# Performance work log

Hardware: AMD Instinct MI355X
Metric: run time of the kernel (lower is better)

Reference implementation:

```python
import jax, jax.numpy as jnp
import numpy as np

VOCAB_SIZES = [100003, 100019, 100043, 100049, 100057, 100069, 100103, 100109,
               100129, 100151, 100153, 100169, 100183, 100189, 100193, 100207]
OFFSETS = np.cumsum([0] + VOCAB_SIZES[:-1]).astype(np.int32)  # per-head offsets into shared table
B, S, G, C = 2, 2048, 4, 2048        # batch, seq, hc_mult branches, base_emb_dim
H, DH = 16, 64                        # total hash heads, dim_per_head
ENGRAM_DIM = H * DH                   # 1024 = num_orders * dim_per_ngram
K, DIL = 4, 3                         # conv kernel_size, dilation = max_ngram_size


def setup_inputs() -> dict:
  key = jax.random.key(0)
  ks = jax.random.split(key, 8)
  total_vocab = sum(VOCAB_SIZES)
  return {
      "hidden_states": jax.random.normal(ks[0], (B, S, G, C), jnp.float32),
      "hash_input_ids": jax.random.randint(ks[1], (B, S, H), 0, min(VOCAB_SIZES), jnp.int32),
      "emb_table": jax.random.normal(ks[2], (total_vocab, DH), jnp.float32) * 0.02,
      "key_w": jax.random.normal(ks[3], (G, ENGRAM_DIM, C), jnp.float32) / np.sqrt(ENGRAM_DIM),
      "key_b": jnp.zeros((G, C), jnp.float32),
      "k_scale": jnp.ones((G, C), jnp.float32) + 0.02 * jax.random.normal(ks[4], (G, C), jnp.float32),
      "q_scale": jnp.ones((G, C), jnp.float32) + 0.02 * jax.random.normal(ks[5], (G, C), jnp.float32),
      "value_w": jax.random.normal(ks[6], (ENGRAM_DIM, C), jnp.float32) / np.sqrt(ENGRAM_DIM),
      "value_b": jnp.zeros((C,), jnp.float32),
      "conv_scale": jnp.ones((G, C), jnp.float32),
      "conv_w": jax.random.normal(ks[7], (K, G * C), jnp.float32) * 0.25,  # depthwise taps
  }


def _rmsnorm(x, scale, eps):
  var = jnp.mean(jnp.square(x), axis=-1, keepdims=True)
  return x * jax.lax.rsqrt(var + eps) * scale


def reference(hidden_states, hash_input_ids, emb_table, key_w, key_b,
              k_scale, q_scale, value_w, value_b, conv_scale, conv_w):
  # 1. Retrieve: offset-shifted multi-head embedding gather
  ids = hash_input_ids + jnp.asarray(OFFSETS)            # (B,S,H)
  emb = emb_table[ids].reshape(B, S, ENGRAM_DIM)         # (B,S,H*DH)
  # 2. Gate: per-branch key projections + RMSNorms, signed-sqrt sigmoid gate
  keys = jnp.einsum('bse,geo->bsgo', emb, key_w) + key_b  # (B,S,G,C)
  k = _rmsnorm(keys, k_scale, 1e-6)
  q = _rmsnorm(hidden_states, q_scale, 1e-6)
  qk = jnp.einsum('bsgc,bsgc->bsg', q, k) / jnp.sqrt(jnp.float32(C))
  gate_logits = jnp.sqrt(jnp.maximum(jnp.abs(qk), 1e-6)) * jnp.sign(qk)
  gates = jax.nn.sigmoid(gate_logits)                    # (B,S,G)
  value = emb @ value_w + value_b                        # (B,S,C)
  v = gates[..., None] * value[:, :, None, :]            # (B,S,G,C)
  # 3. Mix: ShortConv = SiLU(depthwise causal dilated Conv1D(RMSNorm(v)))
  xn = _rmsnorm(v, conv_scale, 1e-5).reshape(B, S, G * C)
  pad = (K - 1) * DIL                                    # causal left pad = 9
  xp = jnp.pad(xn, ((0, 0), (pad, 0), (0, 0)))
  y = sum(xp[:, j * DIL:j * DIL + S, :] * conv_w[j] for j in range(K))
  y = jax.nn.silu(y).reshape(B, S, G, C)
  return v + y
```

## Files before the change

kernel.cpp:

```cpp
#include <hip/hip_runtime.h>
#include <cstdint>
#include <cstddef>

typedef __attribute__((ext_vector_type(8))) __bf16 bf16x8;
typedef __attribute__((ext_vector_type(4))) float f32x4;
typedef __attribute__((ext_vector_type(4))) unsigned short u16x4;
typedef __attribute__((ext_vector_type(8))) unsigned short u16x8;

static constexpr int Bz = 2, Sz = 2048, Gz = 4, Cz = 2048;
static constexpr int Hh = 16, EDz = 1024;
static constexpr int Tz = Bz * Sz;
static constexpr int NALL = Gz * Cz + Cz;

__constant__ int OFF16[16] = {0, 100003, 200022, 300065, 400114, 500171, 600240,
                              700343, 800452, 900581, 1000732, 1100885, 1201054,
                              1301237, 1401426, 1501619};

__device__ __forceinline__ float bf2f(unsigned short s) {
  union { unsigned u; float f; } x; x.u = ((unsigned)s) << 16; return x.f;
}
__device__ __forceinline__ unsigned short f2bf(float f) {
  union { float f; unsigned u; } x; x.f = f;
  unsigned r = x.u + 0x7fff + ((x.u >> 16) & 1);
  return (unsigned short)(r >> 16);
}

__global__ __launch_bounds__(256) void k_bias(const float* __restrict__ key_b,
                                              const float* __restrict__ value_b,
                                              float* __restrict__ bias) {
  int n = blockIdx.x * 256 + threadIdx.x;
  bias[n] = (n < Gz * Cz) ? key_b[n] : value_b[n - Gz * Cz];
}

__global__ __launch_bounds__(256) void k_prepw(const float* __restrict__ key_w,
                                               const float* __restrict__ value_w,
                                               unsigned short* __restrict__ Wt) {
  __shared__ float tile[32][33];
  const int mat = blockIdx.y;
  const int ot = blockIdx.x & 63, kt = blockIdx.x >> 6;
  const float* src = (mat < 4) ? (key_w + (size_t)mat * EDz * Cz) : value_w;
  const int tx = threadIdx.x & 31, ty = threadIdx.x >> 5;
#pragma unroll
  for (int i = 0; i < 4; i++)
    tile[ty + i * 8][tx] = src[(size_t)(kt * 32 + ty + i * 8) * Cz + ot * 32 + tx];
  __syncthreads();
#pragma unroll
  for (int i = 0; i < 4; i++)
    Wt[(size_t)(mat * Cz + ot * 32 + ty + i * 8) * EDz + kt * 32 + tx] =
        f2bf(tile[tx][ty + i * 8]);
}

__global__ __launch_bounds__(256) void k_gather(const int* __restrict__ ids,
                                                const float* __restrict__ table,
                                                unsigned short* __restrict__ emb) {
  const int t = blockIdx.x;
  const int tid = threadIdx.x;
  const int h = tid >> 4;
  const int d = (tid & 15) * 4;
  const long row = (long)(ids[t * Hh + h] + OFF16[h]);
  f32x4 v = *reinterpret_cast<const f32x4*>(table + row * 64 + d);
  u16x4 o;
#pragma unroll
  for (int i = 0; i < 4; i++) o[i] = f2bf(v[i]);
  *reinterpret_cast<u16x4*>(emb + (size_t)t * EDz + tid * 4) = o;
}

#define GEMM_BAR  asm volatile("s_barrier" ::: "memory")
#define GEMM_V4   asm volatile("s_waitcnt vmcnt(4)" ::: "memory")

__global__ __launch_bounds__(512, 2) void k_gemm8(const unsigned short* __restrict__ A,
                                                  const unsigned short* __restrict__ Bw,
                                                  const float* __restrict__ bias,
                                                  unsigned short* __restrict__ Cm) {
  __shared__ unsigned short s_lds[65536];
  char* lds_c = (char*)s_lds;

  const int tid = threadIdx.x;
  const int wid = tid >> 6, lane = tid & 63;
  const int wr = wid >> 2, wc = wid & 3;

  const int bid = blockIdx.x;
  const int swz = (bid & 7) * 80 + (bid >> 3);
  const int bm = swz / 40, bn = swz % 40;
  const int m0 = bm * 256, n0 = bn * 256;

  int rq[2], kq[2];
#pragma unroll
  for (int q = 0; q < 2; q++) {
    int x = q * 8192 + wid * 1024 + lane * 16;
    int y = x ^ (((x >> 9) & 1) << 5);
    rq[q] = ((y >> 11) & 7) * 16 + ((y >> 6) & 15);
    kq[q] = ((y >> 10) & 1) * 32 + ((y >> 1) & 31);
  }
  const int rdb = (((lane & 15) << 6) + ((lane >> 4) << 4)) ^ (((lane >> 3) & 1) << 5);

  const unsigned short* Arow0 = A + (size_t)m0 * EDz;
  const unsigned short* Arow1 = A + (size_t)(m0 + 128) * EDz;
  const unsigned short* Brow0 = Bw + (size_t)n0 * EDz;
  const unsigned short* Brow1 = Bw + (size_t)(n0 + 128) * EDz;

  auto STAGE = [&](const unsigned short* grow, int ldsOff, int kt) {
#pragma unroll
    for (int q = 0; q < 2; q++) {
      const unsigned short* src = grow + (size_t)rq[q] * EDz + kt * 64 + kq[q];
      __builtin_amdgcn_global_load_lds(
          (const __attribute__((address_space(1))) void*)src,
          (__attribute__((address_space(3))) void*)(lds_c + ldsOff + q * 8192 + wid * 1024),
          16, 0, 0);
    }
  };

  f32x4 acc[8][4] = {};
  bf16x8 Af[4][2], Bl[2][2], Bh[2][2];

  auto RD_A = [&](int buf, int msel) {
    const char* p = lds_c + buf * 32768 + wr * 16384 + rdb;
#pragma unroll
    for (int m = 0; m < 4; m++)
#pragma unroll
      for (int ks = 0; ks < 2; ks++)
        Af[m][ks] = *reinterpret_cast<const bf16x8*>(p + (msel * 4 + m) * 2048 + ks * 1024);
  };
  auto RD_B = [&](int buf, int nsel, bf16x8 (&Bf)[2][2]) {
    const char* p = lds_c + 65536 + buf * 32768 + (wc >> 1) * 16384 + (wc & 1) * 8192 + rdb;
#pragma unroll
    for (int n = 0; n < 2; n++)
#pragma unroll
      for (int ks = 0; ks < 2; ks++)
        Bf[n][ks] = *reinterpret_cast<const bf16x8*>(p + (nsel * 2 + n) * 2048 + ks * 1024);
  };
  auto MM = [&](int msel, int nsel, bf16x8 (&Bf)[2][2]) {
    __builtin_amdgcn_s_setprio(1);
#pragma unroll
    for (int m = 0; m < 4; m++)
#pragma unroll
      for (int n = 0; n < 2; n++)
#pragma unroll
        for (int ks = 0; ks < 2; ks++)
          acc[msel * 4 + m][nsel * 2 + n] = __builtin_amdgcn_mfma_f32_16x16x32_bf16(
              Af[m][ks], Bf[n][ks], acc[msel * 4 + m][nsel * 2 + n], 0, 0, 0);
    __builtin_amdgcn_s_setprio(0);
  };

  STAGE(Arow0, 0,             0);
  STAGE(Arow1, 16384,         0);
  STAGE(Brow0, 65536,         0);
  STAGE(Brow1, 65536 + 16384, 0);
  STAGE(Brow0, 65536 + 32768,         1);
  STAGE(Brow1, 65536 + 32768 + 16384, 1);
  GEMM_V4;
  GEMM_BAR;

  for (int i = 0; i < 8; ++i) {
    const int o  = 2 * i + 1;
    const int t2 = (2 * i + 2 > 15) ? 15 : 2 * i + 2;
    const int t3 = (2 * i + 3 > 15) ? 15 : 2 * i + 3;
    RD_A(0, 0); RD_B(0, 0, Bl);
    STAGE(Arow0, 32768, o);
    GEMM_BAR; MM(0, 0, Bl); GEMM_BAR;
    RD_B(0, 1, Bh);
    STAGE(Arow1, 32768 + 16384, o);
    GEMM_BAR; MM(0, 1, Bh); GEMM_BAR;
    RD_A(0, 1);
    STAGE(Brow0, 65536, t2);
    GEMM_BAR; MM(1, 0, Bl); GEMM_BAR;
    STAGE(Brow1, 65536 + 16384, t2);
    GEMM_V4;
    GEMM_BAR; MM(1, 1, Bh); GEMM_BAR;
    RD_A(1, 0); RD_B(1, 0, Bl);
    STAGE(Arow0, 0, t2);
    GEMM_BAR; MM(0, 0, Bl); GEMM_BAR;
    RD_B(1, 1, Bh);
    STAGE(Arow1, 16384, t2);
    GEMM_BAR; MM(0, 1, Bh); GEMM_BAR;
    RD_A(1, 1);
    STAGE(Brow0, 65536 + 32768, t3);
    GEMM_BAR; MM(1, 0, Bl); GEMM_BAR;
    STAGE(Brow1, 65536 + 32768 + 16384, t3);
    GEMM_V4;
    GEMM_BAR; MM(1, 1, Bh); GEMM_BAR;
  }

#pragma unroll
  for (int mrep = 0; mrep < 8; mrep++) {
    const int row = m0 + wr * 128 + mrep * 16 + (lane >> 4) * 4;
#pragma unroll
    for (int nrep = 0; nrep < 4; nrep++) {
      const int col = n0 + wc * 64 + nrep * 16 + (lane & 15);
      const float bb = bias[col];
#pragma unroll
      for (int t = 0; t < 4; t++)
        Cm[(size_t)(row + t) * NALL + col] = f2bf(acc[mrep][nrep][t] + bb);
    }
  }
}

__global__ __launch_bounds__(256) void k_gate(const float* __restrict__ hidden,
                                              const unsigned short* __restrict__ kv,
                                              const float* __restrict__ k_scale,
                                              const float* __restrict__ q_scale,
                                              float* __restrict__ gates,
                                              float* __restrict__ rstd) {
  const int t = blockIdx.x;
  const int tid = threadIdx.x;
  const int lane = tid & 63, w = tid >> 6;
  const int c0 = tid * 8;
  __shared__ float sred[4][13];
  float val[8];
  {
    bf16x8 raw = *reinterpret_cast<const bf16x8*>(kv + (size_t)t * NALL + Gz * Cz + c0);
#pragma unroll
    for (int i = 0; i < 8; i++) val[i] = (float)raw[i];
  }
  float p[13];
#pragma unroll
  for (int j = 0; j < 13; j++) p[j] = 0.f;
#pragma unroll
  for (int i = 0; i < 8; i++) p[12] += val[i] * val[i];
#pragma unroll
  for (int g = 0; g < 4; g++) {
    const float* qp = hidden + (size_t)t * (Gz * Cz) + g * Cz + c0;
    f32x4 q0 = *reinterpret_cast<const f32x4*>(qp);
    f32x4 q1 = *reinterpret_cast<const f32x4*>(qp + 4);
    bf16x8 kr = *reinterpret_cast<const bf16x8*>(kv + (size_t)t * NALL + g * Cz + c0);
    f32x4 qs0 = *reinterpret_cast<const f32x4*>(q_scale + g * Cz + c0);
    f32x4 qs1 = *reinterpret_cast<const f32x4*>(q_scale + g * Cz + c0 + 4);
    f32x4 ks0 = *reinterpret_cast<const f32x4*>(k_scale + g * Cz + c0);
    f32x4 ks1 = *reinterpret_cast<const f32x4*>(k_scale + g * Cz + c0 + 4);
#pragma unroll
    for (int i = 0; i < 8; i++) {
      float qi = (i < 4) ? q0[i] : q1[i - 4];
      float ki = (float)kr[i];
      float qsi = (i < 4) ? qs0[i] : qs1[i - 4];
      float ksi = (i < 4) ? ks0[i] : ks1[i - 4];
      p[3 * g + 0] += qi * qi;
      p[3 * g + 1] += ki * ki;
      p[3 * g + 2] += qi * qsi * ki * ksi;
    }
  }
#pragma unroll
  for (int j = 0; j < 13; j++) {
    float x = p[j];
    for (int off = 32; off; off >>= 1) x += __shfl_down(x, off);
    if (lane == 0) sred[w][j] = x;
  }
  __syncthreads();
  if (tid != 0) return;
  float f[13];
#pragma unroll
  for (int j = 0; j < 13; j++)
    f[j] = sred[0][j] + sred[1][j] + sred[2][j] + sred[3][j];

  const float invC = 1.f / 2048.f;
  const float inv_sqrtC = 0.02209708691f;
  const float msqv = f[12] * invC;
#pragma unroll
  for (int g = 0; g < 4; g++) {
    float rq = rsqrtf(f[3 * g + 0] * invC + 1e-6f);
    float rk = rsqrtf(f[3 * g + 1] * invC + 1e-6f);
    float qk = f[3 * g + 2] * rq * rk * inv_sqrtC;
    float l = sqrtf(fmaxf(fabsf(qk), 1e-6f));
    l = (qk < 0.f) ? -l : l;
    float gate = 1.f / (1.f + expf(-l));
    gates[t * 4 + g] = gate;
    rstd[t * 4 + g] = rsqrtf(gate * gate * msqv + 1e-5f);
  }
}

__global__ __launch_bounds__(256) void k_conv(const unsigned short* __restrict__ kvb,
                                              const float* __restrict__ gates,
                                              const float* __restrict__ rstd,
                                              const float* __restrict__ conv_scale,
                                              const float* __restrict__ conv_w,
                                              float* __restrict__ out) {
  const int th = threadIdx.x;
  const int r = blockIdx.x % 3, seg = blockIdx.x / 3;
  const int bg = blockIdx.y;
  const int b = bg >> 2, g = bg & 3;
  const int c8 = th * 8;
  const int ch = g * Cz + c8;

  float cs[8], w0[8], w1[8], w2[8], w3[8];
#pragma unroll
  for (int q = 0; q < 2; q++) {
    f32x4 a = *reinterpret_cast<const f32x4*>(conv_scale + ch + q * 4);
    f32x4 t0 = *reinterpret_cast<const f32x4*>(conv_w + 0 * 8192 + ch + q * 4);
    f32x4 t1 = *reinterpret_cast<const f32x4*>(conv_w + 1 * 8192 + ch + q * 4);
    f32x4 t2 = *reinterpret_cast<const f32x4*>(conv_w + 2 * 8192 + ch + q * 4);
    f32x4 t3 = *reinterpret_cast<const f32x4*>(conv_w + 3 * 8192 + ch + q * 4);
#pragma unroll
    for (int i = 0; i < 4; i++) {
      cs[q * 4 + i] = a[i];
      w0[q * 4 + i] = t0[i]; w1[q * 4 + i] = t1[i];
      w2[q * 4 + i] = t2[i]; w3[q * 4 + i] = t3[i];
    }
  }

  const int s_begin = seg * 64, s_end = s_begin + 64;
  const int s0 = s_begin + ((r - s_begin) % 3 + 3) % 3;

  float p1[8], p2[8], p3[8];
  auto ldxn = [&](int s, float* dst) {
    if (s < 0) {
#pragma unroll
      for (int i = 0; i < 8; i++) dst[i] = 0.f;
      return;
    }
    const int t = b * Sz + s;
    const float grs = gates[t * 4 + g] * rstd[t * 4 + g];
    u16x8 raw = *reinterpret_cast<const u16x8*>(kvb + (size_t)t * NALL + Gz * Cz + c8);
#pragma unroll
    for (int i = 0; i < 8; i++) dst[i] = bf2f(raw[i]) * grs * cs[i];
  };
  ldxn(s0 - 3, p1); ldxn(s0 - 6, p2); ldxn(s0 - 9, p3);

  for (int s = s0; s < s_end; s += 3) {
    const int t = b * Sz + s;
    const float gate = gates[t * 4 + g];
    const float rsc = rstd[t * 4 + g];
    u16x8 raw = *reinterpret_cast<const u16x8*>(kvb + (size_t)t * NALL + Gz * Cz + c8);
    f32x4 o0, o1;
#pragma unroll
    for (int i = 0; i < 8; i++) {
      float v = bf2f(raw[i]) * gate;
      float xn = v * rsc * cs[i];
      float y = w3[i] * xn + w2[i] * p1[i] + w1[i] * p2[i] + w0[i] * p3[i];
      float sy = y / (1.f + expf(-y));
      float ov = v + sy;
      if (i < 4) o0[i] = ov; else o1[i - 4] = ov;
      p3[i] = p2[i]; p2[i] = p1[i]; p1[i] = xn;
    }
    float* op = out + (size_t)t * (Gz * Cz) + ch;
    *reinterpret_cast<f32x4*>(op) = o0;
    *reinterpret_cast<f32x4*>(op + 4) = o1;
  }
}

extern "C" void kernel_launch(void* const* d_in, const int* in_sizes, int n_in,
                              void* d_out, int out_size, void* d_ws, size_t ws_size,
                              hipStream_t stream) {
  const float* hidden     = (const float*)d_in[0];
  const int*   hashids    = (const int*)d_in[1];
  const float* table      = (const float*)d_in[2];
  const float* key_w      = (const float*)d_in[3];
  const float* key_b      = (const float*)d_in[4];
  const float* k_scale    = (const float*)d_in[5];
  const float* q_scale    = (const float*)d_in[6];
  const float* value_w    = (const float*)d_in[7];
  const float* value_b    = (const float*)d_in[8];
  const float* conv_scale = (const float*)d_in[9];
  const float* conv_w     = (const float*)d_in[10];
  float* out = (float*)d_out;
  char* ws = (char*)d_ws;

  unsigned short* emb = (unsigned short*)(ws + 0);
  unsigned short* Wt  = (unsigned short*)(ws + 8388608);
  unsigned short* kvb = (unsigned short*)(ws + 29360128);
  float* gates = (float*)(ws + 113246208);
  float* rstd  = (float*)(ws + 113311744);
  float* bias  = (float*)(ws + 113377280);

  k_bias<<<dim3(40), dim3(256), 0, stream>>>(key_b, value_b, bias);
  k_prepw<<<dim3(2048, 5), dim3(256), 0, stream>>>(key_w, value_w, Wt);
  k_gather<<<dim3(Tz), dim3(256), 0, stream>>>(hashids, table, emb);
  k_gemm8<<<dim3(640), dim3(512), 0, stream>>>(emb, Wt, bias, kvb);
  k_gate<<<dim3(Tz), dim3(256), 0, stream>>>(hidden, kvb, k_scale, q_scale, gates, rstd);
  k_conv<<<dim3(96, 8), dim3(256), 0, stream>>>(kvb, gates, rstd, conv_scale, conv_w, out);
}
```

Measured before the change: 224.0 us.

## Fuse gate reductions into GEMM epilogue and stop storing key projections

The GEMM epilogue now computes per-token, per-branch partial sums (k², q², q·w·k, v²) directly from the accumulators, reading hidden states there and reducing across lanes with shuffles and global atomics. Only the value projection is written out, as a bf16 buffer. A small finalize kernel turns the sums into gates and rstd. This removes the 64 MB bf16 key write/readback and the separate gate pass, at the cost of atomics, nondeterministic summation order, and hidden-state reads inside the GEMM epilogue.

```diff
diff --git a/kernel.cpp b/kernel.cpp
--- a/kernel.cpp
+++ b/kernel.cpp
@@ -25,11 +25,13 @@
   return (unsigned short)(r >> 16);
 }
 
-__global__ __launch_bounds__(256) void k_bias(const float* __restrict__ key_b,
-                                              const float* __restrict__ value_b,
-                                              float* __restrict__ bias) {
-  int n = blockIdx.x * 256 + threadIdx.x;
-  bias[n] = (n < Gz * Cz) ? key_b[n] : value_b[n - Gz * Cz];
+__global__ __launch_bounds__(256) void k_prep0(const float* __restrict__ q_scale,
+                                               const float* __restrict__ k_scale,
+                                               float* __restrict__ W2,
+                                               float* __restrict__ sums) {
+  int i = blockIdx.x * 256 + threadIdx.x;
+  if (i < 8192) W2[i] = q_scale[i] * k_scale[i];
+  if (i < 53248) sums[i] = 0.f;
 }
 
 __global__ __launch_bounds__(256) void k_prepw(const float* __restrict__ key_w,
@@ -68,10 +70,14 @@
 #define GEMM_BAR  asm volatile("s_barrier" ::: "memory")
 #define GEMM_V4   asm volatile("s_waitcnt vmcnt(4)" ::: "memory")
 
-__global__ __launch_bounds__(512, 2) void k_gemm8(const unsigned short* __restrict__ A,
-                                                  const unsigned short* __restrict__ Bw,
-                                                  const float* __restrict__ bias,
-                                                  unsigned short* __restrict__ Cm) {
+__global__ __launch_bounds__(512, 2) void k_gemm8f(const unsigned short* __restrict__ A,
+                                                   const unsigned short* __restrict__ Bw,
+                                                   const float* __restrict__ hidden,
+                                                   const float* __restrict__ key_b,
+                                                   const float* __restrict__ value_b,
+                                                   const float* __restrict__ W2,
+                                                   float* __restrict__ sums,
+                                                   unsigned short* __restrict__ vbuf) {
   __shared__ unsigned short s_lds[65536];
   char* lds_c = (char*)s_lds;
 
@@ -181,93 +187,99 @@
     GEMM_BAR; MM(1, 1, Bh); GEMM_BAR;
   }
 
-#pragma unroll
-  for (int mrep = 0; mrep < 8; mrep++) {
-    const int row = m0 + wr * 128 + mrep * 16 + (lane >> 4) * 4;
-#pragma unroll
-    for (int nrep = 0; nrep < 4; nrep++) {
-      const int col = n0 + wc * 64 + nrep * 16 + (lane & 15);
-      const float bb = bias[col];
-#pragma unroll
-      for (int t = 0; t < 4; t++)
-        Cm[(size_t)(row + t) * NALL + col] = f2bf(acc[mrep][nrep][t] + bb);
-    }
-  }
-}
-
-__global__ __launch_bounds__(256) void k_gate(const float* __restrict__ hidden,
-                                              const unsigned short* __restrict__ kv,
-                                              const float* __restrict__ k_scale,
-                                              const float* __restrict__ q_scale,
-                                              float* __restrict__ gates,
-                                              float* __restrict__ rstd) {
-  const int t = blockIdx.x;
-  const int tid = threadIdx.x;
-  const int lane = tid & 63, w = tid >> 6;
-  const int c0 = tid * 8;
-  __shared__ float sred[4][13];
-  float val[8];
-  {
-    bf16x8 raw = *reinterpret_cast<const bf16x8*>(kv + (size_t)t * NALL + Gz * Cz + c0);
-#pragma unroll
-    for (int i = 0; i < 8; i++) val[i] = (float)raw[i];
-  }
-  float p[13];
-#pragma unroll
-  for (int j = 0; j < 13; j++) p[j] = 0.f;
-#pragma unroll
-  for (int i = 0; i < 8; i++) p[12] += val[i] * val[i];
-#pragma unroll
-  for (int g = 0; g < 4; g++) {
-    const float* qp = hidden + (size_t)t * (Gz * Cz) + g * Cz + c0;
-    f32x4 q0 = *reinterpret_cast<const f32x4*>(qp);
-    f32x4 q1 = *reinterpret_cast<const f32x4*>(qp + 4);
-    bf16x8 kr = *reinterpret_cast<const bf16x8*>(kv + (size_t)t * NALL + g * Cz + c0);
-    f32x4 qs0 = *reinterpret_cast<const f32x4*>(q_scale + g * Cz + c0);
-    f32x4 qs1 = *reinterpret_cast<const f32x4*>(q_scale + g * Cz + c0 + 4);
-    f32x4 ks0 = *reinterpret_cast<const f32x4*>(k_scale + g * Cz + c0);
-    f32x4 ks1 = *reinterpret_cast<const f32x4*>(k_scale + g * Cz + c0 + 4);
-#pragma unroll
-    for (int i = 0; i < 8; i++) {
-      float qi = (i < 4) ? q0[i] : q1[i - 4];
-      float ki = (float)kr[i];
-      float qsi = (i < 4) ? qs0[i] : qs1[i - 4];
-      float ksi = (i < 4) ? ks0[i] : ks1[i - 4];
-      p[3 * g + 0] += qi * qi;
-      p[3 * g + 1] += ki * ki;
-      p[3 * g + 2] += qi * qsi * ki * ksi;
-    }
-  }
-#pragma unroll
-  for (int j = 0; j < 13; j++) {
-    float x = p[j];
-    for (int off = 32; off; off >>= 1) x += __shfl_down(x, off);
-    if (lane == 0) sred[w][j] = x;
-  }
-  __syncthreads();
-  if (tid != 0) return;
-  float f[13];
-#pragma unroll
-  for (int j = 0; j < 13; j++)
-    f[j] = sred[0][j] + sred[1][j] + sred[2][j] + sred[3][j];
-
+  float* sum_q2  = sums;
+  float* sum_k2  = sums + 16384;
+  float* sum_qwk = sums + 32768;
+  float* sum_v2  = sums + 49152;
+
+  if (n0 < 8192) {
+    const int g = n0 >> 11;
+#pragma unroll
+    for (int mrep = 0; mrep < 8; mrep++) {
+      const int rowb = m0 + wr * 128 + mrep * 16 + (lane >> 4) * 4;
+      float ak2[4] = {0.f, 0.f, 0.f, 0.f};
+      float akq[4] = {0.f, 0.f, 0.f, 0.f};
+      float aq2[4] = {0.f, 0.f, 0.f, 0.f};
+#pragma unroll
+      for (int nrep = 0; nrep < 4; nrep++) {
+        const int col = n0 + wc * 64 + nrep * 16 + (lane & 15);
+        const float kb = key_b[col];
+        const float w2 = W2[col];
+#pragma unroll
+        for (int t = 0; t < 4; t++) {
+          const float k = acc[mrep][nrep][t] + kb;
+          const float h = hidden[(size_t)(rowb + t) * 8192 + col];
+          ak2[t] += k * k;
+          akq[t] += k * h * w2;
+          aq2[t] += h * h;
+        }
+      }
+#pragma unroll
+      for (int t = 0; t < 4; t++) {
+        float a = ak2[t], b = akq[t], c = aq2[t];
+#pragma unroll
+        for (int msk = 1; msk <= 8; msk <<= 1) {
+          a += __shfl_xor(a, msk);
+          b += __shfl_xor(b, msk);
+          c += __shfl_xor(c, msk);
+        }
+        if ((lane & 15) == 0) {
+          const int idx = (rowb + t) * 4 + g;
+          atomicAdd(&sum_k2[idx], a);
+          atomicAdd(&sum_qwk[idx], b);
+          atomicAdd(&sum_q2[idx], c);
+        }
+      }
+    }
+  } else {
+#pragma unroll
+    for (int mrep = 0; mrep < 8; mrep++) {
+      const int rowb = m0 + wr * 128 + mrep * 16 + (lane >> 4) * 4;
+      float av2[4] = {0.f, 0.f, 0.f, 0.f};
+#pragma unroll
+      for (int nrep = 0; nrep < 4; nrep++) {
+        const int vcol = n0 - 8192 + wc * 64 + nrep * 16 + (lane & 15);
+        const float vb = value_b[vcol];
+#pragma unroll
+        for (int t = 0; t < 4; t++) {
+          const float v = acc[mrep][nrep][t] + vb;
+          av2[t] += v * v;
+          vbuf[(size_t)(rowb + t) * 2048 + vcol] = f2bf(v);
+        }
+      }
+#pragma unroll
+      for (int t = 0; t < 4; t++) {
+        float a = av2[t];
+#pragma unroll
+        for (int msk = 1; msk <= 8; msk <<= 1) a += __shfl_xor(a, msk);
+        if ((lane & 15) == 0) atomicAdd(&sum_v2[rowb + t], a);
+      }
+    }
+  }
+}
+
+__global__ __launch_bounds__(256) void k_gatefin(const float* __restrict__ sums,
+                                                 float* __restrict__ gates,
+                                                 float* __restrict__ rstd) {
+  const int i = blockIdx.x * 256 + threadIdx.x;
+  const float* sum_q2  = sums;
+  const float* sum_k2  = sums + 16384;
+  const float* sum_qwk = sums + 32768;
+  const float* sum_v2  = sums + 49152;
+  const int t = i >> 2;
   const float invC = 1.f / 2048.f;
   const float inv_sqrtC = 0.02209708691f;
-  const float msqv = f[12] * invC;
-#pragma unroll
-  for (int g = 0; g < 4; g++) {
-    float rq = rsqrtf(f[3 * g + 0] * invC + 1e-6f);
-    float rk = rsqrtf(f[3 * g + 1] * invC + 1e-6f);
-    float qk = f[3 * g + 2] * rq * rk * inv_sqrtC;
-    float l = sqrtf(fmaxf(fabsf(qk), 1e-6f));
-    l = (qk < 0.f) ? -l : l;
-    float gate = 1.f / (1.f + expf(-l));
-    gates[t * 4 + g] = gate;
-    rstd[t * 4 + g] = rsqrtf(gate * gate * msqv + 1e-5f);
-  }
-}
-
-__global__ __launch_bounds__(256) void k_conv(const unsigned short* __restrict__ kvb,
+  float rqv = rsqrtf(sum_q2[i] * invC + 1e-6f);
+  float rkv = rsqrtf(sum_k2[i] * invC + 1e-6f);
+  float qk = sum_qwk[i] * rqv * rkv * inv_sqrtC;
+  float l = sqrtf(fmaxf(fabsf(qk), 1e-6f));
+  l = (qk < 0.f) ? -l : l;
+  float gate = 1.f / (1.f + expf(-l));
+  gates[i] = gate;
+  rstd[i] = rsqrtf(gate * gate * (sum_v2[t] * invC) + 1e-5f);
+}
+
+__global__ __launch_bounds__(256) void k_conv(const unsigned short* __restrict__ vbuf,
                                               const float* __restrict__ gates,
                                               const float* __restrict__ rstd,
                                               const float* __restrict__ conv_scale,
@@ -308,7 +320,7 @@
     }
     const int t = b * Sz + s;
     const float grs = gates[t * 4 + g] * rstd[t * 4 + g];
-    u16x8 raw = *reinterpret_cast<const u16x8*>(kvb + (size_t)t * NALL + Gz * Cz + c8);
+    u16x8 raw = *reinterpret_cast<const u16x8*>(vbuf + (size_t)t * 2048 + c8);
 #pragma unroll
     for (int i = 0; i < 8; i++) dst[i] = bf2f(raw[i]) * grs * cs[i];
   };
@@ -318,7 +330,7 @@
     const int t = b * Sz + s;
     const float gate = gates[t * 4 + g];
     const float rsc = rstd[t * 4 + g];
-    u16x8 raw = *reinterpret_cast<const u16x8*>(kvb + (size_t)t * NALL + Gz * Cz + c8);
+    u16x8 raw = *reinterpret_cast<const u16x8*>(vbuf + (size_t)t * 2048 + c8);
     f32x4 o0, o1;
 #pragma unroll
     for (int i = 0; i < 8; i++) {
@@ -353,17 +365,19 @@
   float* out = (float*)d_out;
   char* ws = (char*)d_ws;
 
-  unsigned short* emb = (unsigned short*)(ws + 0);
-  unsigned short* Wt  = (unsigned short*)(ws + 8388608);
-  unsigned short* kvb = (unsigned short*)(ws + 29360128);
-  float* gates = (float*)(ws + 113246208);
-  float* rstd  = (float*)(ws + 113311744);
-  float* bias  = (float*)(ws + 113377280);
-
-  k_bias<<<dim3(40), dim3(256), 0, stream>>>(key_b, value_b, bias);
+  unsigned short* emb  = (unsigned short*)(ws + 0);
+  unsigned short* Wt   = (unsigned short*)(ws + 8388608);
+  unsigned short* vbuf = (unsigned short*)(ws + 29360128);
+  float* W2    = (float*)(ws + 46137344);
+  float* sums  = (float*)(ws + 46170112);
+  float* gates = (float*)(ws + 46383104);
+  float* rstd  = (float*)(ws + 46448640);
+
+  k_prep0<<<dim3(208), dim3(256), 0, stream>>>(q_scale, k_scale, W2, sums);
   k_prepw<<<dim3(2048, 5), dim3(256), 0, stream>>>(key_w, value_w, Wt);
   k_gather<<<dim3(Tz), dim3(256), 0, stream>>>(hashids, table, emb);
-  k_gemm8<<<dim3(640), dim3(512), 0, stream>>>(emb, Wt, bias, kvb);
-  k_gate<<<dim3(Tz), dim3(256), 0, stream>>>(hidden, kvb, k_scale, q_scale, gates, rstd);
-  k_conv<<<dim3(96, 8), dim3(256), 0, stream>>>(kvb, gates, rstd, conv_scale, conv_w, out);
-}
+  k_gemm8f<<<dim3(640), dim3(512), 0, stream>>>(emb, Wt, hidden, key_b, value_b,
+                                                W2, sums, vbuf);
+  k_gatefin<<<dim3(64), dim3(256), 0, stream>>>(sums, gates, rstd);
+  k_conv<<<dim3(96, 8), dim3(256), 0, stream>>>(vbuf, gates, rstd, conv_scale, conv_w, out);
+}
```

Result: slower. 363.7 us (+62.4%).
